# Optimization experiments

Hardware: AMD Instinct MI355X
Metric: run time of the kernel (lower is better)

Reference implementation:

```python
import jax, jax.numpy as jnp
import numpy as np

H_FEATS = 256

def setup_inputs() -> dict:
    key = jax.random.key(0)
    k1, k2, k3, k4, k5, k6, k7 = jax.random.split(key, 7)
    N, E, D = 100000, 500000, H_FEATS
    h = jax.random.normal(k1, (N, D), dtype=jnp.float32)
    src = jax.random.randint(k2, (E,), 0, N)
    dst = jax.random.randint(k3, (E,), 0, N)
    # Linear params (PyTorch default init: U(-1/sqrt(fan_in), 1/sqrt(fan_in)))
    b1_bound = 1.0 / np.sqrt(2 * D)
    b2_bound = 1.0 / np.sqrt(D)
    W1 = jax.random.uniform(k4, (2 * D, D), jnp.float32, -b1_bound, b1_bound)
    b1 = jax.random.uniform(k5, (D,), jnp.float32, -b1_bound, b1_bound)
    W2 = jax.random.uniform(k6, (D, 1), jnp.float32, -b2_bound, b2_bound)
    b2 = jax.random.uniform(k7, (1,), jnp.float32, -b2_bound, b2_bound)
    return {"h": h, "src": src, "dst": dst, "W1": W1, "b1": b1, "W2": W2, "b2": b2}

def reference(h, src, dst, W1, b1, W2, b2):
    # Gather per-edge source/destination node features and concat: [E, 2D]
    he = jnp.concatenate([h[src], h[dst]], axis=1)
    # Linear -> ReLU -> (dropout is identity in eval) -> Linear -> Sigmoid
    hid = jax.nn.relu(he @ W1 + b1)          # [E, D]
    score = jax.nn.sigmoid((hid @ W2 + b2).squeeze(1))  # [E]
    return score
```

## Files before the change

### kernel.cpp

```cpp
#include <hip/hip_runtime.h>
#include <math.h>


typedef __attribute__((ext_vector_type(8))) short short8;
typedef __attribute__((ext_vector_type(2))) float floatx2;
typedef __attribute__((ext_vector_type(4))) float floatx4;
typedef __attribute__((ext_vector_type(16))) float floatx16;

#define D_FEAT 256
#define EPW 8

__device__ __forceinline__ float bf2f(unsigned short u) {
    union { unsigned u32; float f; } v; v.u32 = ((unsigned)u) << 16; return v.f;
}
__device__ __forceinline__ float lo16(unsigned u) {
    union { unsigned u32; float f; } v; v.u32 = u << 16; return v.f;
}
__device__ __forceinline__ float hi16(unsigned u) {
    union { unsigned u32; float f; } v; v.u32 = u & 0xffff0000u; return v.f;
}
__device__ __forceinline__ unsigned short f2bf(float f) {
    union { float f; unsigned u32; } v; v.f = f;
    unsigned x = v.u32;
    return (unsigned short)((x + 0x7fffu + ((x >> 16) & 1u)) >> 16);
}
__device__ __forceinline__ float sigmoid_safe(float r) {
    r = fminf(fmaxf(r, -30.f), 30.f);
    return 1.f / (1.f + expf(-r));
}
__device__ __forceinline__ unsigned pack4_fp8(float a, float b, float c, float d) {
    int w = __builtin_amdgcn_cvt_pk_fp8_f32(a, b, 0, false);
    w = __builtin_amdgcn_cvt_pk_fp8_f32(c, d, w, true);
    return (unsigned)w;
}

__global__ __launch_bounds__(256) void probe_dtype(const unsigned short* __restrict__ h,
                                                   int* __restrict__ flag) {
    __shared__ int cnt[256];
    const int t = threadIdx.x;
    int c = 0;
    #pragma unroll
    for (int i = 0; i < 8; ++i) {
        unsigned e = (h[t * 8 + i] >> 7) & 0xFF;
        c += (e >= 100 && e <= 140) ? 1 : 0;
    }
    cnt[t] = c;
    __syncthreads();
    if (t == 0) {
        int s = 0;
        for (int i = 0; i < 256; ++i) s += cnt[i];
        flag[0] = (s >= 1843) ? 1 : 0;
    }
}

template <int MODE>
__global__ __launch_bounds__(256) void build_wt_t(const void* __restrict__ W1v,
                                                  unsigned short* __restrict__ Wt,
                                                  const int* __restrict__ flag) {
    if (flag[0] != MODE) return;
    int j = blockIdx.x, k = threadIdx.x;
    size_t idx = (j < 256) ? ((size_t)k * 256 + j) : ((size_t)(k + 256) * 256 + (j - 256));
    unsigned short v;
    if constexpr (MODE == 1) v = ((const unsigned short*)W1v)[idx];
    else                     v = f2bf(((const float*)W1v)[idx]);
    Wt[(size_t)j * 256 + k] = v;
}

template <int MODE>
__global__ __launch_bounds__(512, 2) void gemm_pq_t(const void* __restrict__ hv,
                                                    const unsigned short* __restrict__ Wt,
                                                    unsigned char* __restrict__ PQ8,
                                                    int N, const int* __restrict__ flag) {
    if (flag[0] != MODE) return;
    __shared__ unsigned short Bs[256][256];
    __shared__ unsigned short As[64][256];

    const int tid  = threadIdx.x;
    const int lane = tid & 63;
    const int wid  = tid >> 6;
    const int l32  = lane & 31;
    const int q2   = lane >> 5;

    {
        const int r = tid >> 1;
        const unsigned cbase = (tid & 1) * 256;
        const char* srcp = (const char*)Wt + (size_t)r * 512 + cbase;
        char* dstb = (char*)&Bs[0][0] + (unsigned)r * 512;
        const unsigned sw = ((unsigned)r & 31) << 4;
        #pragma unroll
        for (int i = 0; i < 16; ++i) {
            short8 v = *(const short8*)(srcp + i * 16);
            *(short8*)(dstb + ((cbase + i * 16) ^ sw)) = v;
        }
    }

    short8 breg[16];
    {
        const char* bp = (const char*)Wt + (size_t)(256 + wid * 32 + l32) * 512 + q2 * 16;
        #pragma unroll
        for (int ks = 0; ks < 16; ++ks)
            breg[ks] = *(const short8*)(bp + ks * 32);
    }

    const int ar = tid >> 3;
    const unsigned ac = (unsigned)(tid & 7) * 64;
    const unsigned aswz = ((unsigned)ar & 31) << 4;

    short8  pref[4];
    floatx4 pf[8];
    auto load_a = [&](int ms) {
        const int gm = ms * 64 + ar;
        if constexpr (MODE == 1) {
            #pragma unroll
            for (int j = 0; j < 4; ++j) {
                short8 v = {};
                if (gm < N)
                    v = *(const short8*)((const char*)hv + (size_t)gm * 512 + ac + j * 16);
                pref[j] = v;
            }
        } else {
            #pragma unroll
            for (int j = 0; j < 4; ++j) {
                floatx4 f0 = {}, f1 = {};
                if (gm < N) {
                    const float* p = (const float*)hv + (size_t)gm * 256 + (ac + j * 16) / 2;
                    f0 = *(const floatx4*)p;
                    f1 = *(const floatx4*)(p + 4);
                }
                pf[2 * j]     = f0;
                pf[2 * j + 1] = f1;
            }
        }
    };

    const int NT = (N + 63) >> 6;
    const int GM = gridDim.x;
    if ((int)blockIdx.x < NT) load_a(blockIdx.x);

    for (int ms = blockIdx.x; ms < NT; ms += GM) {
        __syncthreads();
        {
            char* adst = (char*)&As[0][0] + (unsigned)ar * 512;
            #pragma unroll
            for (int j = 0; j < 4; ++j) {
                short8 v;
                if constexpr (MODE == 1) {
                    v = pref[j];
                } else {
                    floatx4 f0 = pf[2 * j], f1 = pf[2 * j + 1];
                    v[0] = (short)f2bf(f0.x); v[1] = (short)f2bf(f0.y);
                    v[2] = (short)f2bf(f0.z); v[3] = (short)f2bf(f0.w);
                    v[4] = (short)f2bf(f1.x); v[5] = (short)f2bf(f1.y);
                    v[6] = (short)f2bf(f1.z); v[7] = (short)f2bf(f1.w);
                }
                *(short8*)(adst + ((ac + j * 16) ^ aswz)) = v;
            }
        }
        const int msn = ms + GM;
        if (msn < NT) load_a(msn);
        __syncthreads();

        floatx16 acc[2][2] = {};
        #pragma unroll
        for (int ks = 0; ks < 16; ++ks) {
            const unsigned cb = ((unsigned)(ks * 32 + q2 * 16)) ^ ((unsigned)l32 << 4);
            short8 a0 = *(const short8*)((const char*)&As[0][0] + (unsigned)l32 * 512 + cb);
            short8 a1 = *(const short8*)((const char*)&As[0][0] + (unsigned)(32 + l32) * 512 + cb);
            short8 bl = *(const short8*)((const char*)&Bs[0][0] + (unsigned)(wid * 32 + l32) * 512 + cb);
            acc[0][0] = __builtin_amdgcn_mfma_f32_32x32x16_bf16(bl,       a0, acc[0][0], 0, 0, 0);
            acc[1][0] = __builtin_amdgcn_mfma_f32_32x32x16_bf16(bl,       a1, acc[1][0], 0, 0, 0);
            acc[0][1] = __builtin_amdgcn_mfma_f32_32x32x16_bf16(breg[ks], a0, acc[0][1], 0, 0, 0);
            acc[1][1] = __builtin_amdgcn_mfma_f32_32x32x16_bf16(breg[ks], a1, acc[1][1], 0, 0, 0);
        }

        __syncthreads();
        {
            unsigned char* scr = (unsigned char*)&As[0][0];
            #pragma unroll
            for (int mi = 0; mi < 2; ++mi) {
                const unsigned row = (unsigned)(mi * 32 + l32);
                const unsigned rs = (row & 31) << 4;
                #pragma unroll
                for (int nb = 0; nb < 2; ++nb) {
                    const unsigned nbase = (unsigned)(nb * 256 + wid * 32 + 4 * q2);
                    #pragma unroll
                    for (int g = 0; g < 4; ++g) {
                        unsigned w = pack4_fp8(acc[mi][nb][4 * g + 0], acc[mi][nb][4 * g + 1],
                                               acc[mi][nb][4 * g + 2], acc[mi][nb][4 * g + 3]);
                        const unsigned col = nbase + 8 * g;
                        *(unsigned*)(scr + ((row * 512 + col) ^ rs)) = w;
                    }
                }
            }
        }
        __syncthreads();
        {
            const unsigned char* scr = (const unsigned char*)&As[0][0];
            const int gm = ms * 64 + ar;
            if (gm < N) {
                #pragma unroll
                for (int j = 0; j < 4; ++j) {
                    const unsigned col = ac + j * 16;
                    uint4 v = *(const uint4*)(scr + (((unsigned)ar * 512 + col) ^ aswz));
                    *(uint4*)(PQ8 + (size_t)gm * 512 + col) = v;
                }
            }
        }
    }
}

template <int MODE>
__global__ __launch_bounds__(256) void edge_score_t(const unsigned char* __restrict__ PQ8,
                                                    const int* __restrict__ src,
                                                    const int* __restrict__ dst,
                                                    const void* __restrict__ b1v,
                                                    const void* __restrict__ W2v,
                                                    const void* __restrict__ b2v,
                                                    void* __restrict__ outv,
                                                    int E, const int* __restrict__ flag) {
    if (flag[0] != MODE) return;
    const int wave = threadIdx.x >> 6;
    const int lane = threadIdx.x & 63;
    const int e0 = (blockIdx.x * 4 + wave) * EPW;
    if (e0 >= E) return;
    const int l32 = lane & 31;
    const int* __restrict__ idxp = (lane >= 32) ? dst : src;

    float bf[8], wf[8];
    if constexpr (MODE == 1) {
        const uint4 bvr = *(const uint4*)((const unsigned short*)b1v + l32 * 8);
        const uint4 wvr = *(const uint4*)((const unsigned short*)W2v + l32 * 8);
        bf[0] = lo16(bvr.x); bf[1] = hi16(bvr.x); bf[2] = lo16(bvr.y); bf[3] = hi16(bvr.y);
        bf[4] = lo16(bvr.z); bf[5] = hi16(bvr.z); bf[6] = lo16(bvr.w); bf[7] = hi16(bvr.w);
        wf[0] = lo16(wvr.x); wf[1] = hi16(wvr.x); wf[2] = lo16(wvr.y); wf[3] = hi16(wvr.y);
        wf[4] = lo16(wvr.z); wf[5] = hi16(wvr.z); wf[6] = lo16(wvr.w); wf[7] = hi16(wvr.w);
    } else {
        const float* bp = (const float*)b1v + l32 * 8;
        const float* wp = (const float*)W2v + l32 * 8;
        #pragma unroll
        for (int t = 0; t < 8; ++t) { bf[t] = bp[t]; wf[t] = wp[t]; }
    }

    int node[EPW];
    #pragma unroll
    for (int i = 0; i < EPW; ++i) {
        int e = e0 + i; if (e >= E) e = E - 1;
        node[i] = idxp[e];
    }
    uint2 raw[EPW];
    #pragma unroll
    for (int i = 0; i < EPW; ++i)
        raw[i] = *(const uint2*)(PQ8 + (size_t)node[i] * 512 + lane * 8);

    float res[EPW];
    #pragma unroll
    for (int i = 0; i < EPW; ++i) {
        uint2 o;
        o.x = (unsigned)__shfl_xor((int)raw[i].x, 32);
        o.y = (unsigned)__shfl_xor((int)raw[i].y, 32);
        floatx2 p01 = __builtin_amdgcn_cvt_pk_f32_fp8((int)raw[i].x, false);
        floatx2 p23 = __builtin_amdgcn_cvt_pk_f32_fp8((int)raw[i].x, true);
        floatx2 p45 = __builtin_amdgcn_cvt_pk_f32_fp8((int)raw[i].y, false);
        floatx2 p67 = __builtin_amdgcn_cvt_pk_f32_fp8((int)raw[i].y, true);
        floatx2 q01 = __builtin_amdgcn_cvt_pk_f32_fp8((int)o.x, false);
        floatx2 q23 = __builtin_amdgcn_cvt_pk_f32_fp8((int)o.x, true);
        floatx2 q45 = __builtin_amdgcn_cvt_pk_f32_fp8((int)o.y, false);
        floatx2 q67 = __builtin_amdgcn_cvt_pk_f32_fp8((int)o.y, true);
        float v0 = fmaxf(p01.x + q01.x + bf[0], 0.f);
        float v1 = fmaxf(p01.y + q01.y + bf[1], 0.f);
        float v2 = fmaxf(p23.x + q23.x + bf[2], 0.f);
        float v3 = fmaxf(p23.y + q23.y + bf[3], 0.f);
        float v4 = fmaxf(p45.x + q45.x + bf[4], 0.f);
        float v5 = fmaxf(p45.y + q45.y + bf[5], 0.f);
        float v6 = fmaxf(p67.x + q67.x + bf[6], 0.f);
        float v7 = fmaxf(p67.y + q67.y + bf[7], 0.f);
        float sum = v0 * wf[0] + v1 * wf[1] + v2 * wf[2] + v3 * wf[3]
                  + v4 * wf[4] + v5 * wf[5] + v6 * wf[6] + v7 * wf[7];
        #pragma unroll
        for (int off = 1; off <= 16; off <<= 1)
            sum += __shfl_xor(sum, off);
        res[i] = sum;
    }

    if (lane == 0) {
        float bias2;
        if constexpr (MODE == 1) bias2 = bf2f(((const unsigned short*)b2v)[0]);
        else                     bias2 = ((const float*)b2v)[0];
        if constexpr (MODE == 1) {
            union { short8 v; unsigned short u[8]; } r;
            #pragma unroll
            for (int i = 0; i < EPW; ++i)
                r.u[i] = f2bf(sigmoid_safe(res[i] + bias2));
            unsigned short* outp = (unsigned short*)outv;
            if (e0 + EPW <= E) *(short8*)(outp + e0) = r.v;
            else for (int i = 0; i < EPW && e0 + i < E; ++i) outp[e0 + i] = r.u[i];
        } else {
            float* outp = (float*)outv;
            for (int i = 0; i < EPW && e0 + i < E; ++i)
                outp[e0 + i] = sigmoid_safe(res[i] + bias2);
        }
    }
}

template <int MODE>
__global__ __launch_bounds__(256) void edge_fused_t(const void* __restrict__ hv,
                                                    const int* __restrict__ src,
                                                    const int* __restrict__ dst,
                                                    const void* __restrict__ W1v,
                                                    const void* __restrict__ b1v,
                                                    const void* __restrict__ W2v,
                                                    const void* __restrict__ b2v,
                                                    void* __restrict__ outv,
                                                    int E, const int* __restrict__ flag) {
    if (flag && flag[0] != MODE) return;
    __shared__ float he[512];
    __shared__ float wsum[4];
    const int e = blockIdx.x;
    if (e >= E) return;
    const int t = threadIdx.x;
    const int s = src[e];
    const int d = dst[e];

    if constexpr (MODE == 1) {
        he[t]       = bf2f(((const unsigned short*)hv)[(size_t)s * 256 + t]);
        he[256 + t] = bf2f(((const unsigned short*)hv)[(size_t)d * 256 + t]);
    } else {
        he[t]       = ((const float*)hv)[(size_t)s * 256 + t];
        he[256 + t] = ((const float*)hv)[(size_t)d * 256 + t];
    }
    __syncthreads();

    float acc;
    if constexpr (MODE == 1) acc = bf2f(((const unsigned short*)b1v)[t]);
    else                     acc = ((const float*)b1v)[t];

    #pragma unroll 8
    for (int k = 0; k < 512; ++k) {
        float w;
        if constexpr (MODE == 1) w = bf2f(((const unsigned short*)W1v)[(size_t)k * 256 + t]);
        else                     w = ((const float*)W1v)[(size_t)k * 256 + t];
        acc += he[k] * w;
    }

    float w2;
    if constexpr (MODE == 1) w2 = bf2f(((const unsigned short*)W2v)[t]);
    else                     w2 = ((const float*)W2v)[t];
    acc = fmaxf(acc, 0.f) * w2;

    #pragma unroll
    for (int off = 32; off > 0; off >>= 1)
        acc += __shfl_xor(acc, off);
    if ((t & 63) == 0) wsum[t >> 6] = acc;
    __syncthreads();

    if (t == 0) {
        float bias2;
        if constexpr (MODE == 1) bias2 = bf2f(((const unsigned short*)b2v)[0]);
        else                     bias2 = ((const float*)b2v)[0];
        float r = sigmoid_safe(wsum[0] + wsum[1] + wsum[2] + wsum[3] + bias2);
        if constexpr (MODE == 1) ((unsigned short*)outv)[e] = f2bf(r);
        else                     ((float*)outv)[e] = r;
    }
}

extern "C" void kernel_launch(void* const* d_in, const int* in_sizes, int n_in,
                              void* d_out, int out_size, void* d_ws, size_t ws_size,
                              hipStream_t stream) {
    const void* h  = d_in[0];
    const int* src = (const int*)d_in[1];
    const int* dst = (const int*)d_in[2];
    const void* W1 = d_in[3];
    const void* b1 = d_in[4];
    const void* W2 = d_in[5];
    const void* b2 = d_in[6];

    const int N = in_sizes[0] / D_FEAT;
    const int E = in_sizes[1];

    const size_t FLAG_BYTES = 256;
    const size_t wt_bytes  = (size_t)512 * D_FEAT * sizeof(unsigned short);
    const size_t pq_bytes  = (size_t)N * 512;
    const size_t need = FLAG_BYTES + wt_bytes + pq_bytes;

    int* flag = (int*)d_ws;
    unsigned short* Wt = (unsigned short*)((char*)d_ws + FLAG_BYTES);
    unsigned char*  PQ8 = (unsigned char*)((char*)d_ws + FLAG_BYTES + wt_bytes);

    if (ws_size >= need) {
        probe_dtype<<<1, 256, 0, stream>>>((const unsigned short*)h, flag);

        build_wt_t<1><<<512, 256, 0, stream>>>(W1, Wt, flag);
        build_wt_t<0><<<512, 256, 0, stream>>>(W1, Wt, flag);

        gemm_pq_t<1><<<256, 512, 0, stream>>>(h, Wt, PQ8, N, flag);
        gemm_pq_t<0><<<256, 512, 0, stream>>>(h, Wt, PQ8, N, flag);

        int egrid = (E + 4 * EPW - 1) / (4 * EPW);
        edge_score_t<1><<<egrid, 256, 0, stream>>>(PQ8, src, dst, b1, W2, b2, d_out, E, flag);
        edge_score_t<0><<<egrid, 256, 0, stream>>>(PQ8, src, dst, b1, W2, b2, d_out, E, flag);
    } else if (ws_size >= FLAG_BYTES) {
        probe_dtype<<<1, 256, 0, stream>>>((const unsigned short*)h, flag);
        edge_fused_t<1><<<E, 256, 0, stream>>>(h, src, dst, W1, b1, W2, b2, d_out, E, flag);
        edge_fused_t<0><<<E, 256, 0, stream>>>(h, src, dst, W1, b1, W2, b2, d_out, E, flag);
    } else {
        edge_fused_t<1><<<E, 256, 0, stream>>>(h, src, dst, W1, b1, W2, b2, d_out, E, nullptr);
    }
}
```

Before: 264.7 us.

## Keep all W1 B-tiles in registers, double-buffer A in LDS, store PQ8 directly

The node GEMM no longer stages half of W1 in a 128KB LDS buffer. Each wave now holds both of its 32-column B fragments in registers, and the freed LDS becomes a double-buffered A tile. The next tile is written while the current one is consumed, which cuts syncs per iteration from four to one. The FP8 epilogue writes 4-byte chunks straight to global memory instead of going through an LDS transpose, trading coalesced 16-byte stores for fewer barriers. Higher register pressure (32 short8 for B) may hurt occupancy at launch bounds (512,2).

```diff
diff --git a/kernel.cpp b/kernel.cpp
--- a/kernel.cpp
+++ b/kernel.cpp
@@ -72,8 +72,7 @@
                                                     unsigned char* __restrict__ PQ8,
                                                     int N, const int* __restrict__ flag) {
     if (flag[0] != MODE) return;
-    __shared__ unsigned short Bs[256][256];
-    __shared__ unsigned short As[64][256];
+    __shared__ unsigned short As[2][64][256];
 
     const int tid  = threadIdx.x;
     const int lane = tid & 63;
@@ -81,25 +80,15 @@
     const int l32  = lane & 31;
     const int q2   = lane >> 5;
 
+    short8 breg0[16], breg1[16];
     {
-        const int r = tid >> 1;
-        const unsigned cbase = (tid & 1) * 256;
-        const char* srcp = (const char*)Wt + (size_t)r * 512 + cbase;
-        char* dstb = (char*)&Bs[0][0] + (unsigned)r * 512;
-        const unsigned sw = ((unsigned)r & 31) << 4;
-        #pragma unroll
-        for (int i = 0; i < 16; ++i) {
-            short8 v = *(const short8*)(srcp + i * 16);
-            *(short8*)(dstb + ((cbase + i * 16) ^ sw)) = v;
-        }
-    }
-
-    short8 breg[16];
-    {
-        const char* bp = (const char*)Wt + (size_t)(256 + wid * 32 + l32) * 512 + q2 * 16;
-        #pragma unroll
-        for (int ks = 0; ks < 16; ++ks)
-            breg[ks] = *(const short8*)(bp + ks * 32);
+        const char* bp0 = (const char*)Wt + (size_t)(wid * 64 + l32) * 512 + q2 * 16;
+        const char* bp1 = bp0 + 32 * 512;
+        #pragma unroll
+        for (int ks = 0; ks < 16; ++ks) {
+            breg0[ks] = *(const short8*)(bp0 + ks * 32);
+            breg1[ks] = *(const short8*)(bp1 + ks * 32);
+        }
     }
 
     const int ar = tid >> 3;
@@ -132,80 +121,71 @@
             }
         }
     };
+    auto write_a = [&](int p) {
+        char* adst = (char*)&As[p][0][0] + (unsigned)ar * 512;
+        #pragma unroll
+        for (int j = 0; j < 4; ++j) {
+            short8 v;
+            if constexpr (MODE == 1) {
+                v = pref[j];
+            } else {
+                floatx4 f0 = pf[2 * j], f1 = pf[2 * j + 1];
+                v[0] = (short)f2bf(f0.x); v[1] = (short)f2bf(f0.y);
+                v[2] = (short)f2bf(f0.z); v[3] = (short)f2bf(f0.w);
+                v[4] = (short)f2bf(f1.x); v[5] = (short)f2bf(f1.y);
+                v[6] = (short)f2bf(f1.z); v[7] = (short)f2bf(f1.w);
+            }
+            *(short8*)(adst + ((ac + j * 16) ^ aswz)) = v;
+        }
+    };
 
     const int NT = (N + 63) >> 6;
     const int GM = gridDim.x;
-    if ((int)blockIdx.x < NT) load_a(blockIdx.x);
-
-    for (int ms = blockIdx.x; ms < NT; ms += GM) {
-        __syncthreads();
-        {
-            char* adst = (char*)&As[0][0] + (unsigned)ar * 512;
-            #pragma unroll
-            for (int j = 0; j < 4; ++j) {
-                short8 v;
-                if constexpr (MODE == 1) {
-                    v = pref[j];
-                } else {
-                    floatx4 f0 = pf[2 * j], f1 = pf[2 * j + 1];
-                    v[0] = (short)f2bf(f0.x); v[1] = (short)f2bf(f0.y);
-                    v[2] = (short)f2bf(f0.z); v[3] = (short)f2bf(f0.w);
-                    v[4] = (short)f2bf(f1.x); v[5] = (short)f2bf(f1.y);
-                    v[6] = (short)f2bf(f1.z); v[7] = (short)f2bf(f1.w);
-                }
-                *(short8*)(adst + ((ac + j * 16) ^ aswz)) = v;
-            }
-        }
-        const int msn = ms + GM;
-        if (msn < NT) load_a(msn);
-        __syncthreads();
+    const int bid = blockIdx.x;
+
+    load_a(bid);
+    write_a(0);
+    if (bid + GM < NT) load_a(bid + GM);
+    __syncthreads();
+
+    int p = 0;
+    for (int ms = bid; ms < NT; ms += GM) {
+        write_a(p ^ 1);
+        if (ms + 2 * GM < NT) load_a(ms + 2 * GM);
 
         floatx16 acc[2][2] = {};
+        const char* abase = (const char*)&As[p][0][0];
         #pragma unroll
         for (int ks = 0; ks < 16; ++ks) {
             const unsigned cb = ((unsigned)(ks * 32 + q2 * 16)) ^ ((unsigned)l32 << 4);
-            short8 a0 = *(const short8*)((const char*)&As[0][0] + (unsigned)l32 * 512 + cb);
-            short8 a1 = *(const short8*)((const char*)&As[0][0] + (unsigned)(32 + l32) * 512 + cb);
-            short8 bl = *(const short8*)((const char*)&Bs[0][0] + (unsigned)(wid * 32 + l32) * 512 + cb);
-            acc[0][0] = __builtin_amdgcn_mfma_f32_32x32x16_bf16(bl,       a0, acc[0][0], 0, 0, 0);
-            acc[1][0] = __builtin_amdgcn_mfma_f32_32x32x16_bf16(bl,       a1, acc[1][0], 0, 0, 0);
-            acc[0][1] = __builtin_amdgcn_mfma_f32_32x32x16_bf16(breg[ks], a0, acc[0][1], 0, 0, 0);
-            acc[1][1] = __builtin_amdgcn_mfma_f32_32x32x16_bf16(breg[ks], a1, acc[1][1], 0, 0, 0);
-        }
-
-        __syncthreads();
-        {
-            unsigned char* scr = (unsigned char*)&As[0][0];
-            #pragma unroll
-            for (int mi = 0; mi < 2; ++mi) {
-                const unsigned row = (unsigned)(mi * 32 + l32);
-                const unsigned rs = (row & 31) << 4;
+            short8 a0 = *(const short8*)(abase + (unsigned)l32 * 512 + cb);
+            short8 a1 = *(const short8*)(abase + (unsigned)(32 + l32) * 512 + cb);
+            acc[0][0] = __builtin_amdgcn_mfma_f32_32x32x16_bf16(breg0[ks], a0, acc[0][0], 0, 0, 0);
+            acc[1][0] = __builtin_amdgcn_mfma_f32_32x32x16_bf16(breg0[ks], a1, acc[1][0], 0, 0, 0);
+            acc[0][1] = __builtin_amdgcn_mfma_f32_32x32x16_bf16(breg1[ks], a0, acc[0][1], 0, 0, 0);
+            acc[1][1] = __builtin_amdgcn_mfma_f32_32x32x16_bf16(breg1[ks], a1, acc[1][1], 0, 0, 0);
+        }
+
+        const int m_base = ms * 64;
+        #pragma unroll
+        for (int mi = 0; mi < 2; ++mi) {
+            int m = m_base + mi * 32 + l32;
+            if (m < N) {
                 #pragma unroll
                 for (int nb = 0; nb < 2; ++nb) {
-                    const unsigned nbase = (unsigned)(nb * 256 + wid * 32 + 4 * q2);
+                    int cbase = wid * 64 + nb * 32 + 4 * q2;
                     #pragma unroll
                     for (int g = 0; g < 4; ++g) {
                         unsigned w = pack4_fp8(acc[mi][nb][4 * g + 0], acc[mi][nb][4 * g + 1],
                                                acc[mi][nb][4 * g + 2], acc[mi][nb][4 * g + 3]);
-                        const unsigned col = nbase + 8 * g;
-                        *(unsigned*)(scr + ((row * 512 + col) ^ rs)) = w;
+                        *(unsigned*)(PQ8 + (size_t)m * 512 + cbase + 8 * g) = w;
                     }
                 }
             }
         }
+
         __syncthreads();
-        {
-            const unsigned char* scr = (const unsigned char*)&As[0][0];
-            const int gm = ms * 64 + ar;
-            if (gm < N) {
-                #pragma unroll
-                for (int j = 0; j < 4; ++j) {
-                    const unsigned col = ac + j * 16;
-                    uint4 v = *(const uint4*)(scr + (((unsigned)ar * 512 + col) ^ aswz));
-                    *(uint4*)(PQ8 + (size_t)gm * 512 + col) = v;
-                }
-            }
-        }
+        p ^= 1;
     }
 }
 
```

After: 284.6 us. +7.5%, slower.

## Process 16 edges per wave with transpose-style butterfly reduction

Applied to the files above, without the earlier changes.

Doubles edges per wave from 8 to 16 so more independent row gathers are in flight per wave. It replaces the per-edge 5-step shuffle reduction with a recursive-halving butterfly that reduces 16 partial sums across lanes using fewer total shuffles. Lanes 0-15 then each compute the sigmoid and write one output instead of lane 0 doing all of them. Register pressure rises with 16 raw loads held at once, which may reduce occupancy, and there are half as many waves for latency hiding.

```diff
diff --git a/kernel.cpp b/kernel.cpp
--- a/kernel.cpp
+++ b/kernel.cpp
@@ -8,7 +8,7 @@
 typedef __attribute__((ext_vector_type(16))) float floatx16;
 
 #define D_FEAT 256
-#define EPW 8
+#define EPW 16
 
 __device__ __forceinline__ float bf2f(unsigned short u) {
     union { unsigned u32; float f; } v; v.u32 = ((unsigned)u) << 16; return v.f;
@@ -240,6 +240,9 @@
         #pragma unroll
         for (int t = 0; t < 8; ++t) { bf[t] = bp[t]; wf[t] = wp[t]; }
     }
+    float bias2;
+    if constexpr (MODE == 1) bias2 = bf2f(((const unsigned short*)b2v)[0]);
+    else                     bias2 = ((const float*)b2v)[0];
 
     int node[EPW];
     #pragma unroll
@@ -274,30 +277,49 @@
         float v5 = fmaxf(p45.y + q45.y + bf[5], 0.f);
         float v6 = fmaxf(p67.x + q67.x + bf[6], 0.f);
         float v7 = fmaxf(p67.y + q67.y + bf[7], 0.f);
-        float sum = v0 * wf[0] + v1 * wf[1] + v2 * wf[2] + v3 * wf[3]
-                  + v4 * wf[4] + v5 * wf[5] + v6 * wf[6] + v7 * wf[7];
-        #pragma unroll
-        for (int off = 1; off <= 16; off <<= 1)
-            sum += __shfl_xor(sum, off);
-        res[i] = sum;
-    }
-
-    if (lane == 0) {
-        float bias2;
-        if constexpr (MODE == 1) bias2 = bf2f(((const unsigned short*)b2v)[0]);
-        else                     bias2 = ((const float*)b2v)[0];
-        if constexpr (MODE == 1) {
-            union { short8 v; unsigned short u[8]; } r;
-            #pragma unroll
-            for (int i = 0; i < EPW; ++i)
-                r.u[i] = f2bf(sigmoid_safe(res[i] + bias2));
-            unsigned short* outp = (unsigned short*)outv;
-            if (e0 + EPW <= E) *(short8*)(outp + e0) = r.v;
-            else for (int i = 0; i < EPW && e0 + i < E; ++i) outp[e0 + i] = r.u[i];
-        } else {
-            float* outp = (float*)outv;
-            for (int i = 0; i < EPW && e0 + i < E; ++i)
-                outp[e0 + i] = sigmoid_safe(res[i] + bias2);
+        res[i] = v0 * wf[0] + v1 * wf[1] + v2 * wf[2] + v3 * wf[3]
+               + v4 * wf[4] + v5 * wf[5] + v6 * wf[6] + v7 * wf[7];
+    }
+
+    float t8[8];
+    #pragma unroll
+    for (int k = 0; k < 8; ++k) {
+        float a = res[2 * k], b = res[2 * k + 1];
+        float own  = (lane & 1) ? b : a;
+        float send = (lane & 1) ? a : b;
+        t8[k] = own + __shfl_xor(send, 1);
+    }
+    float t4[4];
+    #pragma unroll
+    for (int k = 0; k < 4; ++k) {
+        float a = t8[2 * k], b = t8[2 * k + 1];
+        float own  = (lane & 2) ? b : a;
+        float send = (lane & 2) ? a : b;
+        t4[k] = own + __shfl_xor(send, 2);
+    }
+    float t2[2];
+    #pragma unroll
+    for (int k = 0; k < 2; ++k) {
+        float a = t4[2 * k], b = t4[2 * k + 1];
+        float own  = (lane & 4) ? b : a;
+        float send = (lane & 4) ? a : b;
+        t2[k] = own + __shfl_xor(send, 4);
+    }
+    float t1;
+    {
+        float a = t2[0], b = t2[1];
+        float own  = (lane & 8) ? b : a;
+        float send = (lane & 8) ? a : b;
+        t1 = own + __shfl_xor(send, 8);
+    }
+    t1 += __shfl_xor(t1, 16);
+
+    if (lane < 16) {
+        const int e = e0 + lane;
+        if (e < E) {
+            float r = sigmoid_safe(t1 + bias2);
+            if constexpr (MODE == 1) ((unsigned short*)outv)[e] = f2bf(r);
+            else                     ((float*)outv)[e] = r;
         }
     }
 }
```

New measurement: 247.6 us. 6.4% less time.
